# Kernel tuning notes

Hardware: AMD Instinct MI355X
Metric: run time of the kernel (lower is better)

Reference implementation:

```python
import jax, jax.numpy as jnp
import numpy as np

D_MODEL = 1024
NHEADS = 16
D_K = D_MODEL // NHEADS


def setup_inputs() -> dict:
    key = jax.random.key(0)
    ks = jax.random.split(key, 5)
    s = 1.0 / np.sqrt(D_MODEL)
    x = jax.random.normal(ks[0], (4, 2048, D_MODEL), dtype=jnp.float32)
    Wq = jax.random.normal(ks[1], (D_MODEL, D_MODEL), dtype=jnp.float32) * s
    Wk = jax.random.normal(ks[2], (D_MODEL, D_MODEL), dtype=jnp.float32) * s
    Wv = jax.random.normal(ks[3], (D_MODEL, D_MODEL), dtype=jnp.float32) * s
    Wo = jax.random.normal(ks[4], (D_MODEL, D_MODEL), dtype=jnp.float32) * s
    z = jnp.zeros((D_MODEL,), dtype=jnp.float32)
    return {"x": x, "Wq": Wq, "bq": z, "Wk": Wk, "bk": z,
            "Wv": Wv, "bv": z, "Wo": Wo, "bo": z}


def reference(x, Wq, bq, Wk, bk, Wv, bv, Wo, bo):
    B, S, _ = x.shape
    # nn.Linear: y = x @ W^T + b  (weights stored [out, in])
    def proj(W, b):
        h = x @ W.T + b                       # [B, S, D]
        return h.reshape(B, S, NHEADS, D_K).transpose(0, 2, 1, 3)  # [B, H, S, d_k]
    Q = proj(Wq, bq)
    K = proj(Wk, bk)
    V = proj(Wv, bv)
    scores = jnp.einsum("bhqd,bhkd->bhqk", Q, K) / jnp.sqrt(jnp.float32(D_K))
    attn = jax.nn.softmax(scores, axis=-1)    # dropout p=0.0 -> identity
    ctx = jnp.einsum("bhqk,bhkd->bhqd", attn, V)
    ctx = ctx.transpose(0, 2, 1, 3).reshape(B, S, D_MODEL)
    return ctx @ Wo.T + bo
```

## Files before the change

### kernel.cpp

```cpp
#include <hip/hip_runtime.h>
#include <stdint.h>
#include <stddef.h>

typedef _Float16 f16;
typedef f16 f16x8 __attribute__((ext_vector_type(8)));
typedef f16 f16x4 __attribute__((ext_vector_type(4)));
typedef f16 f16x2 __attribute__((ext_vector_type(2)));
typedef float f32x4 __attribute__((ext_vector_type(4)));
typedef float f32x16 __attribute__((ext_vector_type(16)));
typedef unsigned int u32x4 __attribute__((ext_vector_type(4)));

#define SEQ 2048
#define DM 1024
#define NH 16
#define DK 64
#define MTOT 8192

__device__ __forceinline__ void gload16(const f16* g, f16* l) {
    __builtin_amdgcn_global_load_lds(
        (const __attribute__((address_space(1))) uint32_t*)g,
        (__attribute__((address_space(3))) uint32_t*)l,
        16, 0, 0);
}

__device__ __forceinline__ unsigned int pkrtz(float a, float b) {
    return __builtin_bit_cast(unsigned int, __builtin_amdgcn_cvt_pkrtz(a, b));
}

__device__ __forceinline__ void plswap(unsigned int& a, unsigned int& b) {
    auto r = __builtin_amdgcn_permlane32_swap(a, b, false, false);
    unsigned int n0 = r[0], n1 = r[1];
    a = n0; b = n1;
}
__device__ __forceinline__ float xhalf_sum(float x) {
    unsigned int ux = __builtin_bit_cast(unsigned int, x);
    auto r = __builtin_amdgcn_permlane32_swap(ux, ux, false, false);
    unsigned int n0 = r[0], n1 = r[1];
    return __builtin_bit_cast(float, n0) + __builtin_bit_cast(float, n1);
}

__global__ void cvt_f32_f16(const float* __restrict__ src, f16* __restrict__ dst, int n) {
    int i = (blockIdx.x * 256 + threadIdx.x) * 8;
    if (i >= n) return;
    float4 a = *(const float4*)(src + i);
    float4 b = *(const float4*)(src + i + 4);
    f16x8 o = {(f16)a.x, (f16)a.y, (f16)a.z, (f16)a.w,
               (f16)b.x, (f16)b.y, (f16)b.z, (f16)b.w};
    *(f16x8*)(dst + i) = o;
}

__global__ void cvt4(const float* __restrict__ s0, const float* __restrict__ s1,
                     const float* __restrict__ s2, const float* __restrict__ s3,
                     f16* __restrict__ d0, f16* __restrict__ d1,
                     f16* __restrict__ d2, f16* __restrict__ d3) {
    int y = blockIdx.y;
    const float* s = y == 0 ? s0 : y == 1 ? s1 : y == 2 ? s2 : s3;
    f16* d = y == 0 ? d0 : y == 1 ? d1 : y == 2 ? d2 : d3;
    int i = (blockIdx.x * 256 + threadIdx.x) * 8;
    float4 a = *(const float4*)(s + i);
    float4 b = *(const float4*)(s + i + 4);
    f16x8 o = {(f16)a.x, (f16)a.y, (f16)a.z, (f16)a.w,
               (f16)b.x, (f16)b.y, (f16)b.z, (f16)b.w};
    *(f16x8*)(d + i) = o;
}

__device__ __forceinline__
void gemm_body(const f16* __restrict__ A, const f16* __restrict__ Bw,
               const float* __restrict__ bias, void* __restrict__ outp,
               int mode, float oscale, int bm, int bn, f16* As, f16* Bs) {
    const int tid = threadIdx.x;
    const int w = tid >> 6, lane = tid & 63;
    const int g = lane >> 4, c16 = lane & 15;
    const int wr = w >> 1, wc = w & 1;
    const int r8 = lane >> 3, co = (lane & 7) * 8;

    f32x4 acc[4][4] = {};

    const f16* Ab = A + (size_t)bm * 128 * DM;
    const f16* Bb = Bw + (size_t)bn * 128 * DM;

    for (int kt = 0; kt < DM / 64; ++kt) {
        if (kt) __syncthreads();
        const f16* As_src = Ab + kt * 64;
        const f16* Bs_src = Bb + kt * 64;
#pragma unroll
        for (int i = 0; i < 4; ++i) {
            int c = 4 * w + i;
            gload16(As_src + (size_t)(c * 8 + r8) * DM + co, As + c * 512);
            gload16(Bs_src + (size_t)(c * 8 + r8) * DM + co, Bs + c * 512);
        }
        __syncthreads();
#pragma unroll
        for (int kk = 0; kk < 2; ++kk) {
            f16x8 a[4], b[4];
            const int ko = kk * 32 + g * 8;
#pragma unroll
            for (int m = 0; m < 4; ++m)
                a[m] = *(const f16x8*)(As + (wr * 64 + m * 16 + c16) * 64 + ko);
#pragma unroll
            for (int n = 0; n < 4; ++n)
                b[n] = *(const f16x8*)(Bs + (wc * 64 + n * 16 + c16) * 64 + ko);
#pragma unroll
            for (int m = 0; m < 4; ++m)
#pragma unroll
                for (int n = 0; n < 4; ++n)
                    acc[m][n] = __builtin_amdgcn_mfma_f32_16x16x32_f16(a[m], b[n], acc[m][n], 0, 0, 0);
        }
    }

#pragma unroll
    for (int m = 0; m < 4; ++m) {
#pragma unroll
        for (int n = 0; n < 4; ++n) {
            const int col = bn * 128 + wc * 64 + n * 16 + c16;
            const float bv = bias[col];
            const int row0 = bm * 128 + wr * 64 + m * 16 + g * 4;
            if (mode == 1) {
                int b = row0 >> 11, s0 = row0 & 2047;
                int h = col >> 6, d = col & 63;
                f16x4 pv;
#pragma unroll
                for (int j = 0; j < 4; ++j) pv[j] = (f16)((acc[m][n][j] + bv) * oscale);
                *(f16x4*)((f16*)outp + (((size_t)(b * NH + h) * DK + d) * SEQ + s0)) = pv;
            } else if (mode == 0) {
#pragma unroll
                for (int j = 0; j < 4; ++j) {
                    int row = row0 + j;
                    int b = row >> 11, s = row & 2047;
                    int h = col >> 6, d = col & 63;
                    ((f16*)outp)[((size_t)(b * NH + h) * SEQ + s) * DK + d] =
                        (f16)((acc[m][n][j] + bv) * oscale);
                }
            } else {
#pragma unroll
                for (int j = 0; j < 4; ++j) {
                    int row = row0 + j;
                    ((float*)outp)[(size_t)row * DM + col] = acc[m][n][j] + bv;
                }
            }
        }
    }
}

__global__ __launch_bounds__(256, 2)
void gemm_qkv(const f16* __restrict__ A,
              const f16* __restrict__ W0, const f16* __restrict__ W1, const f16* __restrict__ W2,
              const float* __restrict__ b0, const float* __restrict__ b1, const float* __restrict__ b2,
              f16* __restrict__ Qo, f16* __restrict__ Ko, f16* __restrict__ Vto) {
    __shared__ __align__(16) f16 As[128 * 64];
    __shared__ __align__(16) f16 Bs[128 * 64];
    const int bid = blockIdx.x;
    const int wg = (bid & 7) * 192 + (bid >> 3);
    const int which = wg >> 9;
    const int t = wg & 511;
    const f16* Bw = which == 0 ? W0 : which == 1 ? W1 : W2;
    const float* bias = which == 0 ? b0 : which == 1 ? b1 : b2;
    void* outp = which == 0 ? (void*)Qo : which == 1 ? (void*)Ko : (void*)Vto;
    const int mode = (which == 2) ? 1 : 0;
    const float oscale = (which == 0) ? 0.18033688f : 1.0f;
    gemm_body(A, Bw, bias, outp, mode, oscale, t >> 3, t & 7, As, Bs);
}

__global__ __launch_bounds__(256, 2)
void gemm_out(const f16* __restrict__ A, const f16* __restrict__ Wo,
              const float* __restrict__ bias, float* __restrict__ outp) {
    __shared__ __align__(16) f16 As[128 * 64];
    __shared__ __align__(16) f16 Bs[128 * 64];
    const int bid = blockIdx.x;
    const int wg = (bid & 7) * 64 + (bid >> 3);
    gemm_body(A, Wo, bias, outp, 2, 1.0f, wg >> 3, wg & 7, As, Bs);
}

__global__ __launch_bounds__(256, 2)
void attn(const f16* __restrict__ Qg, const f16* __restrict__ Kg,
          const f16* __restrict__ Vg, f16* __restrict__ ctx) {
    __shared__ __align__(16) f16 Ks[2][64 * 64];
    __shared__ __align__(16) f16 Vs[2][64 * 64];
    const int tid = threadIdx.x;
    const int w = tid >> 6, lane = tid & 63;
    const int q31 = lane & 31, hi = lane >> 5;
    const int bid = blockIdx.x;
    const int wg = (bid & 7) * 64 + (bid >> 3);
    const int bh = wg >> 3, qt = wg & 7;
    const int b = bh >> 4, h = bh & 15;
    const f16* Qp = Qg + (size_t)bh * SEQ * DK;
    const f16* Kp = Kg + (size_t)bh * SEQ * DK;
    const f16* Vp = Vg + (size_t)bh * DK * SEQ;
    const int q0w = qt * 256 + w * 64;

    f16x8 qfA[4], qfB[4];
#pragma unroll
    for (int ks4 = 0; ks4 < 4; ++ks4) {
        qfA[ks4] = *(const f16x8*)(Qp + (size_t)(q0w + q31) * DK + ks4 * 16 + hi * 8);
        qfB[ks4] = *(const f16x8*)(Qp + (size_t)(q0w + 32 + q31) * DK + ks4 * 16 + hi * 8);
    }

    const f32x16 z = {};
    const f16x2 one2 = {(f16)1.0f, (f16)1.0f};
    f32x16 OA0 = {}, OA1 = {}, OB0 = {}, OB1 = {};
    float lrA = 0.f, lrB = 0.f;

    const int srow = lane >> 3;
    const int scol = lane & 7;

#define STAGE(bufi, kvoff)                                                        \
    {                                                                             \
        _Pragma("unroll")                                                         \
        for (int i_ = 0; i_ < 2; ++i_) {                                          \
            int c_ = w * 2 + i_;                                                  \
            int row_ = c_ * 8 + srow;                                             \
            int csw_ = (scol ^ (row_ & 7)) * 8;                                   \
            gload16(Kp + (size_t)((kvoff) + row_) * DK + csw_, &Ks[bufi][c_ * 512]); \
            gload16(Vp + (size_t)row_ * SEQ + (kvoff) + csw_, &Vs[bufi][c_ * 512]);  \
        }                                                                         \
    }

    STAGE(0, 0);
    __syncthreads();
    int cur = 0;
    const int fsw = (q31 & 7) << 4;

    auto soft32 = [&](f32x16& sp, f16x8& paLo, f16x8& paHi, float& ls) {
#pragma unroll
        for (int r = 0; r < 16; ++r) sp[r] = __builtin_amdgcn_exp2f(sp[r]);
        unsigned int u[8];
#pragma unroll
        for (int j = 0; j < 4; ++j) {
            u[2 * j]     = pkrtz(sp[4 * j], sp[4 * j + 1]);
            u[2 * j + 1] = pkrtz(sp[4 * j + 2], sp[4 * j + 3]);
        }
        float ls0 = 0.f, ls1 = 0.f;
#pragma unroll
        for (int j = 0; j < 4; ++j) {
            ls0 = __builtin_amdgcn_fdot2(__builtin_bit_cast(f16x2, u[2 * j]), one2, ls0, false);
            ls1 = __builtin_amdgcn_fdot2(__builtin_bit_cast(f16x2, u[2 * j + 1]), one2, ls1, false);
        }
        ls += ls0 + ls1;
        plswap(u[0], u[2]);
        plswap(u[1], u[3]);
        plswap(u[4], u[6]);
        plswap(u[5], u[7]);
        u32x4 t0w = {u[0], u[1], u[2], u[3]};
        u32x4 t1w = {u[4], u[5], u[6], u[7]};
        paLo = __builtin_bit_cast(f16x8, t0w);
        paHi = __builtin_bit_cast(f16x8, t1w);
    };

    for (int kv = 0; kv < SEQ; kv += 64) {
        if (kv + 64 < SEQ) STAGE(cur ^ 1, kv + 64);

        const char* Kb = (const char*)Ks[cur];
        const char* Vb = (const char*)Vs[cur];
        f32x16 sA0, sA1, sB0, sB1;

#pragma unroll
        for (int ks4 = 0; ks4 < 4; ++ks4) {
            const int off = (ks4 * 32 + hi * 16) ^ fsw;
            f16x8 kf0 = *(const f16x8*)(Kb + q31 * 128 + off);
            if (ks4 == 0) {
                sA0 = __builtin_amdgcn_mfma_f32_32x32x16_f16(kf0, qfA[0], z, 0, 0, 0);
                sB0 = __builtin_amdgcn_mfma_f32_32x32x16_f16(kf0, qfB[0], z, 0, 0, 0);
            } else {
                sA0 = __builtin_amdgcn_mfma_f32_32x32x16_f16(kf0, qfA[ks4], sA0, 0, 0, 0);
                sB0 = __builtin_amdgcn_mfma_f32_32x32x16_f16(kf0, qfB[ks4], sB0, 0, 0, 0);
            }
        }
#pragma unroll
        for (int ks4 = 0; ks4 < 4; ++ks4) {
            const int off = (ks4 * 32 + hi * 16) ^ fsw;
            f16x8 kf1 = *(const f16x8*)(Kb + (32 + q31) * 128 + off);
            if (ks4 == 0) {
                sA1 = __builtin_amdgcn_mfma_f32_32x32x16_f16(kf1, qfA[0], z, 0, 0, 0);
                sB1 = __builtin_amdgcn_mfma_f32_32x32x16_f16(kf1, qfB[0], z, 0, 0, 0);
            } else {
                sA1 = __builtin_amdgcn_mfma_f32_32x32x16_f16(kf1, qfA[ks4], sA1, 0, 0, 0);
                sB1 = __builtin_amdgcn_mfma_f32_32x32x16_f16(kf1, qfB[ks4], sB1, 0, 0, 0);
            }
        }

        f16x8 paA[4], paB[4];
        float lsA = 0.f, lsB = 0.f;

        soft32(sA0, paA[0], paA[1], lsA);
        soft32(sB0, paB[0], paB[1], lsB);

#pragma unroll
        for (int ksl = 0; ksl < 2; ++ksl) {
            const int off = (ksl * 32 + hi * 16) ^ fsw;
            f16x8 vf0 = *(const f16x8*)(Vb + q31 * 128 + off);
            f16x8 vf1 = *(const f16x8*)(Vb + (32 + q31) * 128 + off);
            OA0 = __builtin_amdgcn_mfma_f32_32x32x16_f16(vf0, paA[ksl], OA0, 0, 0, 0);
            OA1 = __builtin_amdgcn_mfma_f32_32x32x16_f16(vf1, paA[ksl], OA1, 0, 0, 0);
            OB0 = __builtin_amdgcn_mfma_f32_32x32x16_f16(vf0, paB[ksl], OB0, 0, 0, 0);
            OB1 = __builtin_amdgcn_mfma_f32_32x32x16_f16(vf1, paB[ksl], OB1, 0, 0, 0);
        }

        soft32(sA1, paA[2], paA[3], lsA);
        soft32(sB1, paB[2], paB[3], lsB);

#pragma unroll
        for (int ksl = 2; ksl < 4; ++ksl) {
            const int off = (ksl * 32 + hi * 16) ^ fsw;
            f16x8 vf0 = *(const f16x8*)(Vb + q31 * 128 + off);
            f16x8 vf1 = *(const f16x8*)(Vb + (32 + q31) * 128 + off);
            OA0 = __builtin_amdgcn_mfma_f32_32x32x16_f16(vf0, paA[ksl], OA0, 0, 0, 0);
            OA1 = __builtin_amdgcn_mfma_f32_32x32x16_f16(vf1, paA[ksl], OA1, 0, 0, 0);
            OB0 = __builtin_amdgcn_mfma_f32_32x32x16_f16(vf0, paB[ksl], OB0, 0, 0, 0);
            OB1 = __builtin_amdgcn_mfma_f32_32x32x16_f16(vf1, paB[ksl], OB1, 0, 0, 0);
        }

        lrA += xhalf_sum(lsA);
        lrB += xhalf_sum(lsB);

        __syncthreads();
        cur ^= 1;
    }
#undef STAGE

    f16* tw = (f16*)&Ks[0][0] + w * 4096;
    {
        const float rlA = 1.f / lrA;
        const float rlB = 1.f / lrB;
#pragma unroll
        for (int f = 0; f < 2; ++f) {
            const float rl = f ? rlB : rlA;
            char* twf = (char*)tw + f * 4096;
#pragma unroll
            for (int dblk = 0; dblk < 2; ++dblk) {
                const f32x16& Op = f ? (dblk ? OB1 : OB0) : (dblk ? OA1 : OA0);
#pragma unroll
                for (int rp = 0; rp < 8; ++rp) {
                    int r = 2 * rp;
                    int d0 = dblk * 32 + (r & 3) + 8 * (r >> 2) + 4 * hi;
                    unsigned int uv = pkrtz(Op[r] * rl, Op[r + 1] * rl);
                    *(unsigned int*)(twf + q31 * 128 + ((d0 * 2) ^ ((q31 & 7) << 4))) = uv;
                }
            }
        }
    }
#pragma unroll
    for (int p4 = 0; p4 < 8; ++p4) {
        int qq = p4 * 8 + (lane >> 3), ch = lane & 7;
        f16x8 v = *(const f16x8*)((const char*)tw + (qq >> 5) * 4096 + (qq & 31) * 128 +
                                  ((ch * 16) ^ ((qq & 7) << 4)));
        *(f16x8*)(ctx + (size_t)(b * SEQ + q0w + qq) * DM + h * DK + ch * 8) = v;
    }
}

extern "C" void kernel_launch(void* const* d_in, const int* in_sizes, int n_in,
                              void* d_out, int out_size, void* d_ws, size_t ws_size,
                              hipStream_t stream) {
    const float* x  = (const float*)d_in[0];
    const float* Wq = (const float*)d_in[1];
    const float* bq = (const float*)d_in[2];
    const float* Wk = (const float*)d_in[3];
    const float* bk = (const float*)d_in[4];
    const float* Wv = (const float*)d_in[5];
    const float* bv = (const float*)d_in[6];
    const float* Wo = (const float*)d_in[7];
    const float* bo = (const float*)d_in[8];

    f16* ws  = (f16*)d_ws;
    f16* xh  = ws;
    f16* Wqh = ws + (size_t)8 * 1024 * 1024;
    f16* Wkh = Wqh + 1024 * 1024;
    f16* Wvh = Wkh + 1024 * 1024;
    f16* Woh = Wvh + 1024 * 1024;
    f16* Vtb = Woh + 1024 * 1024;
    f16* Qb = (f16*)d_out;
    f16* Kb = Qb + (size_t)8 * 1024 * 1024;
    f16* ctx = xh;

    const int nx = MTOT * DM;
    cvt_f32_f16<<<nx / 8 / 256, 256, 0, stream>>>(x, xh, nx);
    cvt4<<<dim3(512, 4), 256, 0, stream>>>(Wq, Wk, Wv, Wo, Wqh, Wkh, Wvh, Woh);

    gemm_qkv<<<1536, 256, 0, stream>>>(xh, Wqh, Wkh, Wvh, bq, bk, bv, Qb, Kb, Vtb);

    attn<<<512, 256, 0, stream>>>(Qb, Kb, Vtb, ctx);

    gemm_out<<<512, 256, 0, stream>>>(ctx, Woh, bo, (float*)d_out);
}
```

Measured before the change: 190.1 us.

## Software-pipeline attention loop with 4-deep KV ring and QK lookahead

Restructures the attention inner loop so the QK^T MFMAs for the next KV tile are issued while the softmax and PV MFMAs of the current tile run, using a 4-buffer LDS ring with prefetch two tiles ahead and explicit vmcnt waits plus raw barriers. It also moves the cross-half row-sum reduction out of the loop to the end. This aims to hide exp/pack latency and global-load latency behind matrix work, at the cost of doubled LDS usage (64 KB per block) and more live score registers, which may reduce occupancy.

```diff
diff --git a/kernel.cpp b/kernel.cpp
--- a/kernel.cpp
+++ b/kernel.cpp
@@ -174,8 +174,8 @@
 __global__ __launch_bounds__(256, 2)
 void attn(const f16* __restrict__ Qg, const f16* __restrict__ Kg,
           const f16* __restrict__ Vg, f16* __restrict__ ctx) {
-    __shared__ __align__(16) f16 Ks[2][64 * 64];
-    __shared__ __align__(16) f16 Vs[2][64 * 64];
+    __shared__ __align__(16) f16 Ks[4][64 * 64];
+    __shared__ __align__(16) f16 Vs[4][64 * 64];
     const int tid = threadIdx.x;
     const int w = tid >> 6, lane = tid & 63;
     const int q31 = lane & 31, hi = lane >> 5;
@@ -195,13 +195,13 @@
         qfB[ks4] = *(const f16x8*)(Qp + (size_t)(q0w + 32 + q31) * DK + ks4 * 16 + hi * 8);
     }
 
-    const f32x16 z = {};
     const f16x2 one2 = {(f16)1.0f, (f16)1.0f};
     f32x16 OA0 = {}, OA1 = {}, OB0 = {}, OB1 = {};
     float lrA = 0.f, lrB = 0.f;
 
     const int srow = lane >> 3;
     const int scol = lane & 7;
+    const int fsw = (q31 & 7) << 4;
 
 #define STAGE(bufi, kvoff)                                                        \
     {                                                                             \
@@ -215,12 +215,19 @@
         }                                                                         \
     }
 
-    STAGE(0, 0);
-    __syncthreads();
-    int cur = 0;
-    const int fsw = (q31 & 7) << 4;
-
-    auto soft32 = [&](f32x16& sp, f16x8& paLo, f16x8& paHi, float& ls) {
+    auto qk32 = [&](const char* Kb, int base, f32x16& sA, f32x16& sB) {
+        sA = (f32x16){};
+        sB = (f32x16){};
+#pragma unroll
+        for (int ks4 = 0; ks4 < 4; ++ks4) {
+            const int off = (ks4 * 32 + hi * 16) ^ fsw;
+            f16x8 kf = *(const f16x8*)(Kb + (base + q31) * 128 + off);
+            sA = __builtin_amdgcn_mfma_f32_32x32x16_f16(kf, qfA[ks4], sA, 0, 0, 0);
+            sB = __builtin_amdgcn_mfma_f32_32x32x16_f16(kf, qfB[ks4], sB, 0, 0, 0);
+        }
+    };
+
+    auto soft32 = [&](f32x16& sp, f16x8& paLo, f16x8& paHi, float& lr) {
 #pragma unroll
         for (int r = 0; r < 16; ++r) sp[r] = __builtin_amdgcn_exp2f(sp[r]);
         unsigned int u[8];
@@ -235,7 +242,7 @@
             ls0 = __builtin_amdgcn_fdot2(__builtin_bit_cast(f16x2, u[2 * j]), one2, ls0, false);
             ls1 = __builtin_amdgcn_fdot2(__builtin_bit_cast(f16x2, u[2 * j + 1]), one2, ls1, false);
         }
-        ls += ls0 + ls1;
+        lr += ls0 + ls1;
         plswap(u[0], u[2]);
         plswap(u[1], u[3]);
         plswap(u[4], u[6]);
@@ -246,46 +253,9 @@
         paHi = __builtin_bit_cast(f16x8, t1w);
     };
 
-    for (int kv = 0; kv < SEQ; kv += 64) {
-        if (kv + 64 < SEQ) STAGE(cur ^ 1, kv + 64);
-
-        const char* Kb = (const char*)Ks[cur];
-        const char* Vb = (const char*)Vs[cur];
-        f32x16 sA0, sA1, sB0, sB1;
-
-#pragma unroll
-        for (int ks4 = 0; ks4 < 4; ++ks4) {
-            const int off = (ks4 * 32 + hi * 16) ^ fsw;
-            f16x8 kf0 = *(const f16x8*)(Kb + q31 * 128 + off);
-            if (ks4 == 0) {
-                sA0 = __builtin_amdgcn_mfma_f32_32x32x16_f16(kf0, qfA[0], z, 0, 0, 0);
-                sB0 = __builtin_amdgcn_mfma_f32_32x32x16_f16(kf0, qfB[0], z, 0, 0, 0);
-            } else {
-                sA0 = __builtin_amdgcn_mfma_f32_32x32x16_f16(kf0, qfA[ks4], sA0, 0, 0, 0);
-                sB0 = __builtin_amdgcn_mfma_f32_32x32x16_f16(kf0, qfB[ks4], sB0, 0, 0, 0);
-            }
-        }
-#pragma unroll
-        for (int ks4 = 0; ks4 < 4; ++ks4) {
-            const int off = (ks4 * 32 + hi * 16) ^ fsw;
-            f16x8 kf1 = *(const f16x8*)(Kb + (32 + q31) * 128 + off);
-            if (ks4 == 0) {
-                sA1 = __builtin_amdgcn_mfma_f32_32x32x16_f16(kf1, qfA[0], z, 0, 0, 0);
-                sB1 = __builtin_amdgcn_mfma_f32_32x32x16_f16(kf1, qfB[0], z, 0, 0, 0);
-            } else {
-                sA1 = __builtin_amdgcn_mfma_f32_32x32x16_f16(kf1, qfA[ks4], sA1, 0, 0, 0);
-                sB1 = __builtin_amdgcn_mfma_f32_32x32x16_f16(kf1, qfB[ks4], sB1, 0, 0, 0);
-            }
-        }
-
-        f16x8 paA[4], paB[4];
-        float lsA = 0.f, lsB = 0.f;
-
-        soft32(sA0, paA[0], paA[1], lsA);
-        soft32(sB0, paB[0], paB[1], lsB);
-
-#pragma unroll
-        for (int ksl = 0; ksl < 2; ++ksl) {
+    auto pv = [&](const char* Vb, f16x8* paA, f16x8* paB) {
+#pragma unroll
+        for (int ksl = 0; ksl < 4; ++ksl) {
             const int off = (ksl * 32 + hi * 16) ^ fsw;
             f16x8 vf0 = *(const f16x8*)(Vb + q31 * 128 + off);
             f16x8 vf1 = *(const f16x8*)(Vb + (32 + q31) * 128 + off);
@@ -294,33 +264,52 @@
             OB0 = __builtin_amdgcn_mfma_f32_32x32x16_f16(vf0, paB[ksl], OB0, 0, 0, 0);
             OB1 = __builtin_amdgcn_mfma_f32_32x32x16_f16(vf1, paB[ksl], OB1, 0, 0, 0);
         }
-
-        soft32(sA1, paA[2], paA[3], lsA);
-        soft32(sB1, paB[2], paB[3], lsB);
-
-#pragma unroll
-        for (int ksl = 2; ksl < 4; ++ksl) {
-            const int off = (ksl * 32 + hi * 16) ^ fsw;
-            f16x8 vf0 = *(const f16x8*)(Vb + q31 * 128 + off);
-            f16x8 vf1 = *(const f16x8*)(Vb + (32 + q31) * 128 + off);
-            OA0 = __builtin_amdgcn_mfma_f32_32x32x16_f16(vf0, paA[ksl], OA0, 0, 0, 0);
-            OA1 = __builtin_amdgcn_mfma_f32_32x32x16_f16(vf1, paA[ksl], OA1, 0, 0, 0);
-            OB0 = __builtin_amdgcn_mfma_f32_32x32x16_f16(vf0, paB[ksl], OB0, 0, 0, 0);
-            OB1 = __builtin_amdgcn_mfma_f32_32x32x16_f16(vf1, paB[ksl], OB1, 0, 0, 0);
-        }
-
-        lrA += xhalf_sum(lsA);
-        lrB += xhalf_sum(lsB);
-
-        __syncthreads();
-        cur ^= 1;
-    }
+    };
+
+    STAGE(0, 0);
+    STAGE(1, 64);
+    asm volatile("s_waitcnt vmcnt(4)" ::: "memory");
+    __builtin_amdgcn_s_barrier();
+    __builtin_amdgcn_sched_barrier(0);
+
+    f32x16 sEA0, sEA1, sEB0, sEB1;
+    f32x16 sOA0, sOA1, sOB0, sOB1;
+    qk32((const char*)Ks[0], 0, sEA0, sEB0);
+    qk32((const char*)Ks[0], 32, sEA1, sEB1);
+
+#define ITER(t, cA0, cA1, cB0, cB1, nA0, nA1, nB0, nB1)                           \
+    {                                                                             \
+        if ((t) + 2 < 32) STAGE(((t) + 2) & 3, ((t) + 2) * 64);                   \
+        f16x8 paA[4], paB[4];                                                     \
+        soft32(cA0, paA[0], paA[1], lrA);               \
+        soft32(cB0, paB[0], paB[1], lrB);                                         \
+        if ((t) + 1 < 32) {                                                       \
+            if ((t) + 2 < 32) asm volatile("s_waitcnt vmcnt(4)" ::: "memory");    \
+            else              asm volatile("s_waitcnt vmcnt(0)" ::: "memory");    \
+            __builtin_amdgcn_s_barrier();                                         \
+            __builtin_amdgcn_sched_barrier(0);                                    \
+            const char* Kn = (const char*)Ks[((t) + 1) & 3];                      \
+            qk32(Kn, 0, nA0, nB0);                           \
+            qk32(Kn, 32, nA1, nB1);                                               \
+        }                                                                         \
+        soft32(cA1, paA[2], paA[3], lrA);             \
+        soft32(cB1, paB[2], paB[3], lrB);                                         \
+        pv((const char*)Vs[(t) & 3], paA, paB);                                   \
+    }
+
+    for (int t = 0; t < 32; t += 2) {
+        ITER(t,     sEA0, sEA1, sEB0, sEB1, sOA0, sOA1, sOB0, sOB1);
+        ITER(t + 1, sOA0, sOA1, sOB0, sOB1, sEA0, sEA1, sEB0, sEB1);
+    }
+#undef ITER
 #undef STAGE
+
+    __syncthreads();
 
     f16* tw = (f16*)&Ks[0][0] + w * 4096;
     {
-        const float rlA = 1.f / lrA;
-        const float rlB = 1.f / lrB;
+        const float rlA = 1.f / xhalf_sum(lrA);
+        const float rlB = 1.f / xhalf_sum(lrB);
 #pragma unroll
         for (int f = 0; f < 2; ++f) {
             const float rl = f ? rlB : rlA;
```

Result: slower. 310.3 us, median of 2 (+63.2%).

## Load K/V fragments directly from global in attention; merge conversion kernels

Applied to the files above, without the earlier changes.

The attention kernel drops its double-buffered LDS staging of K and V tiles and the per-iteration barrier. Each wave now reads K and V MFMA fragments straight from global memory, relying on L1/L2 to absorb the reuse across the four waves. The two f32-to-f16 conversion launches are also merged into one kernel to save a launch. The risk is that uncoalesced or redundant global loads per wave raise memory latency and traffic in the inner loop, since there is no longer explicit prefetch overlap.

```diff
diff --git a/kernel.cpp b/kernel.cpp
--- a/kernel.cpp
+++ b/kernel.cpp
@@ -39,24 +39,25 @@
     return __builtin_bit_cast(float, n0) + __builtin_bit_cast(float, n1);
 }
 
-__global__ void cvt_f32_f16(const float* __restrict__ src, f16* __restrict__ dst, int n) {
-    int i = (blockIdx.x * 256 + threadIdx.x) * 8;
-    if (i >= n) return;
-    float4 a = *(const float4*)(src + i);
-    float4 b = *(const float4*)(src + i + 4);
-    f16x8 o = {(f16)a.x, (f16)a.y, (f16)a.z, (f16)a.w,
-               (f16)b.x, (f16)b.y, (f16)b.z, (f16)b.w};
-    *(f16x8*)(dst + i) = o;
-}
-
-__global__ void cvt4(const float* __restrict__ s0, const float* __restrict__ s1,
-                     const float* __restrict__ s2, const float* __restrict__ s3,
-                     f16* __restrict__ d0, f16* __restrict__ d1,
-                     f16* __restrict__ d2, f16* __restrict__ d3) {
-    int y = blockIdx.y;
-    const float* s = y == 0 ? s0 : y == 1 ? s1 : y == 2 ? s2 : s3;
-    f16* d = y == 0 ? d0 : y == 1 ? d1 : y == 2 ? d2 : d3;
-    int i = (blockIdx.x * 256 + threadIdx.x) * 8;
+__global__ void cvt_all(const float* __restrict__ x,
+                        const float* __restrict__ w0, const float* __restrict__ w1,
+                        const float* __restrict__ w2, const float* __restrict__ w3,
+                        f16* __restrict__ xh,
+                        f16* __restrict__ d0, f16* __restrict__ d1,
+                        f16* __restrict__ d2, f16* __restrict__ d3) {
+    int bid = blockIdx.x;
+    const float* s;
+    f16* d;
+    int off;
+    if (bid < 4096) { s = x; d = xh; off = bid; }
+    else {
+        int t = bid - 4096;
+        int which = t >> 9;
+        off = t & 511;
+        s = which == 0 ? w0 : which == 1 ? w1 : which == 2 ? w2 : w3;
+        d = which == 0 ? d0 : which == 1 ? d1 : which == 2 ? d2 : d3;
+    }
+    int i = (off * 256 + threadIdx.x) * 8;
     float4 a = *(const float4*)(s + i);
     float4 b = *(const float4*)(s + i + 4);
     f16x8 o = {(f16)a.x, (f16)a.y, (f16)a.z, (f16)a.w,
@@ -174,8 +175,7 @@
 __global__ __launch_bounds__(256, 2)
 void attn(const f16* __restrict__ Qg, const f16* __restrict__ Kg,
           const f16* __restrict__ Vg, f16* __restrict__ ctx) {
-    __shared__ __align__(16) f16 Ks[2][64 * 64];
-    __shared__ __align__(16) f16 Vs[2][64 * 64];
+    __shared__ __align__(16) f16 TW[4][4096];
     const int tid = threadIdx.x;
     const int w = tid >> 6, lane = tid & 63;
     const int q31 = lane & 31, hi = lane >> 5;
@@ -200,26 +200,6 @@
     f32x16 OA0 = {}, OA1 = {}, OB0 = {}, OB1 = {};
     float lrA = 0.f, lrB = 0.f;
 
-    const int srow = lane >> 3;
-    const int scol = lane & 7;
-
-#define STAGE(bufi, kvoff)                                                        \
-    {                                                                             \
-        _Pragma("unroll")                                                         \
-        for (int i_ = 0; i_ < 2; ++i_) {                                          \
-            int c_ = w * 2 + i_;                                                  \
-            int row_ = c_ * 8 + srow;                                             \
-            int csw_ = (scol ^ (row_ & 7)) * 8;                                   \
-            gload16(Kp + (size_t)((kvoff) + row_) * DK + csw_, &Ks[bufi][c_ * 512]); \
-            gload16(Vp + (size_t)row_ * SEQ + (kvoff) + csw_, &Vs[bufi][c_ * 512]);  \
-        }                                                                         \
-    }
-
-    STAGE(0, 0);
-    __syncthreads();
-    int cur = 0;
-    const int fsw = (q31 & 7) << 4;
-
     auto soft32 = [&](f32x16& sp, f16x8& paLo, f16x8& paHi, float& ls) {
 #pragma unroll
         for (int r = 0; r < 16; ++r) sp[r] = __builtin_amdgcn_exp2f(sp[r]);
@@ -246,35 +226,32 @@
         paHi = __builtin_bit_cast(f16x8, t1w);
     };
 
+    const f16* Krow0 = Kp + (size_t)q31 * DK + hi * 8;
+    const f16* Krow1 = Kp + (size_t)(32 + q31) * DK + hi * 8;
+    const f16* Vrow0 = Vp + (size_t)q31 * SEQ + hi * 8;
+    const f16* Vrow1 = Vp + (size_t)(32 + q31) * SEQ + hi * 8;
+
     for (int kv = 0; kv < SEQ; kv += 64) {
-        if (kv + 64 < SEQ) STAGE(cur ^ 1, kv + 64);
-
-        const char* Kb = (const char*)Ks[cur];
-        const char* Vb = (const char*)Vs[cur];
         f32x16 sA0, sA1, sB0, sB1;
 
-#pragma unroll
-        for (int ks4 = 0; ks4 < 4; ++ks4) {
-            const int off = (ks4 * 32 + hi * 16) ^ fsw;
-            f16x8 kf0 = *(const f16x8*)(Kb + q31 * 128 + off);
-            if (ks4 == 0) {
-                sA0 = __builtin_amdgcn_mfma_f32_32x32x16_f16(kf0, qfA[0], z, 0, 0, 0);
-                sB0 = __builtin_amdgcn_mfma_f32_32x32x16_f16(kf0, qfB[0], z, 0, 0, 0);
-            } else {
-                sA0 = __builtin_amdgcn_mfma_f32_32x32x16_f16(kf0, qfA[ks4], sA0, 0, 0, 0);
-                sB0 = __builtin_amdgcn_mfma_f32_32x32x16_f16(kf0, qfB[ks4], sB0, 0, 0, 0);
-            }
-        }
-#pragma unroll
-        for (int ks4 = 0; ks4 < 4; ++ks4) {
-            const int off = (ks4 * 32 + hi * 16) ^ fsw;
-            f16x8 kf1 = *(const f16x8*)(Kb + (32 + q31) * 128 + off);
-            if (ks4 == 0) {
-                sA1 = __builtin_amdgcn_mfma_f32_32x32x16_f16(kf1, qfA[0], z, 0, 0, 0);
-                sB1 = __builtin_amdgcn_mfma_f32_32x32x16_f16(kf1, qfB[0], z, 0, 0, 0);
-            } else {
-                sA1 = __builtin_amdgcn_mfma_f32_32x32x16_f16(kf1, qfA[ks4], sA1, 0, 0, 0);
-                sB1 = __builtin_amdgcn_mfma_f32_32x32x16_f16(kf1, qfB[ks4], sB1, 0, 0, 0);
+        {
+            const f16* K0 = Krow0 + (size_t)kv * DK;
+            const f16* K1 = Krow1 + (size_t)kv * DK;
+#pragma unroll
+            for (int ks4 = 0; ks4 < 4; ++ks4) {
+                f16x8 kf0 = *(const f16x8*)(K0 + ks4 * 16);
+                f16x8 kf1 = *(const f16x8*)(K1 + ks4 * 16);
+                if (ks4 == 0) {
+                    sA0 = __builtin_amdgcn_mfma_f32_32x32x16_f16(kf0, qfA[0], z, 0, 0, 0);
+                    sB0 = __builtin_amdgcn_mfma_f32_32x32x16_f16(kf0, qfB[0], z, 0, 0, 0);
+                    sA1 = __builtin_amdgcn_mfma_f32_32x32x16_f16(kf1, qfA[0], z, 0, 0, 0);
+                    sB1 = __builtin_amdgcn_mfma_f32_32x32x16_f16(kf1, qfB[0], z, 0, 0, 0);
+                } else {
+                    sA0 = __builtin_amdgcn_mfma_f32_32x32x16_f16(kf0, qfA[ks4], sA0, 0, 0, 0);
+                    sB0 = __builtin_amdgcn_mfma_f32_32x32x16_f16(kf0, qfB[ks4], sB0, 0, 0, 0);
+                    sA1 = __builtin_amdgcn_mfma_f32_32x32x16_f16(kf1, qfA[ks4], sA1, 0, 0, 0);
+                    sB1 = __builtin_amdgcn_mfma_f32_32x32x16_f16(kf1, qfB[ks4], sB1, 0, 0, 0);
+                }
             }
         }
 
@@ -283,41 +260,28 @@
 
         soft32(sA0, paA[0], paA[1], lsA);
         soft32(sB0, paB[0], paB[1], lsB);
-
-#pragma unroll
-        for (int ksl = 0; ksl < 2; ++ksl) {
-            const int off = (ksl * 32 + hi * 16) ^ fsw;
-            f16x8 vf0 = *(const f16x8*)(Vb + q31 * 128 + off);
-            f16x8 vf1 = *(const f16x8*)(Vb + (32 + q31) * 128 + off);
-            OA0 = __builtin_amdgcn_mfma_f32_32x32x16_f16(vf0, paA[ksl], OA0, 0, 0, 0);
-            OA1 = __builtin_amdgcn_mfma_f32_32x32x16_f16(vf1, paA[ksl], OA1, 0, 0, 0);
-            OB0 = __builtin_amdgcn_mfma_f32_32x32x16_f16(vf0, paB[ksl], OB0, 0, 0, 0);
-            OB1 = __builtin_amdgcn_mfma_f32_32x32x16_f16(vf1, paB[ksl], OB1, 0, 0, 0);
-        }
-
         soft32(sA1, paA[2], paA[3], lsA);
         soft32(sB1, paB[2], paB[3], lsB);
 
-#pragma unroll
-        for (int ksl = 2; ksl < 4; ++ksl) {
-            const int off = (ksl * 32 + hi * 16) ^ fsw;
-            f16x8 vf0 = *(const f16x8*)(Vb + q31 * 128 + off);
-            f16x8 vf1 = *(const f16x8*)(Vb + (32 + q31) * 128 + off);
-            OA0 = __builtin_amdgcn_mfma_f32_32x32x16_f16(vf0, paA[ksl], OA0, 0, 0, 0);
-            OA1 = __builtin_amdgcn_mfma_f32_32x32x16_f16(vf1, paA[ksl], OA1, 0, 0, 0);
-            OB0 = __builtin_amdgcn_mfma_f32_32x32x16_f16(vf0, paB[ksl], OB0, 0, 0, 0);
-            OB1 = __builtin_amdgcn_mfma_f32_32x32x16_f16(vf1, paB[ksl], OB1, 0, 0, 0);
+        {
+            const f16* V0 = Vrow0 + kv;
+            const f16* V1 = Vrow1 + kv;
+#pragma unroll
+            for (int ksl = 0; ksl < 4; ++ksl) {
+                f16x8 vf0 = *(const f16x8*)(V0 + ksl * 16);
+                f16x8 vf1 = *(const f16x8*)(V1 + ksl * 16);
+                OA0 = __builtin_amdgcn_mfma_f32_32x32x16_f16(vf0, paA[ksl], OA0, 0, 0, 0);
+                OA1 = __builtin_amdgcn_mfma_f32_32x32x16_f16(vf1, paA[ksl], OA1, 0, 0, 0);
+                OB0 = __builtin_amdgcn_mfma_f32_32x32x16_f16(vf0, paB[ksl], OB0, 0, 0, 0);
+                OB1 = __builtin_amdgcn_mfma_f32_32x32x16_f16(vf1, paB[ksl], OB1, 0, 0, 0);
+            }
         }
 
         lrA += xhalf_sum(lsA);
         lrB += xhalf_sum(lsB);
-
-        __syncthreads();
-        cur ^= 1;
-    }
-#undef STAGE
-
-    f16* tw = (f16*)&Ks[0][0] + w * 4096;
+    }
+
+    f16* tw = &TW[w][0];
     {
         const float rlA = 1.f / lrA;
         const float rlB = 1.f / lrB;
@@ -371,9 +335,7 @@
     f16* Kb = Qb + (size_t)8 * 1024 * 1024;
     f16* ctx = xh;
 
-    const int nx = MTOT * DM;
-    cvt_f32_f16<<<nx / 8 / 256, 256, 0, stream>>>(x, xh, nx);
-    cvt4<<<dim3(512, 4), 256, 0, stream>>>(Wq, Wk, Wv, Wo, Wqh, Wkh, Wvh, Woh);
+    cvt_all<<<4096 + 4 * 512, 256, 0, stream>>>(x, Wq, Wk, Wv, Wo, xh, Wqh, Wkh, Wvh, Woh);
 
     gemm_qkv<<<1536, 256, 0, stream>>>(xh, Wqh, Wkh, Wvh, bq, bk, bv, Qb, Kb, Vtb);
 
```

Result: slower. 229.1 us, median of 2 (+20.5%).
